# Kernel optimization log

Measured on AMD Instinct MI355X. Metric: run time of the kernel, lower is better.

Reference implementation:

```python
import jax, jax.numpy as jnp
import numpy as np

NEG_SLOPE = 0.01  # torch F.leaky_relu default


def _gcn_conv(x, edge_index, Wc, bc):
    """PyG GCNConv with add_self_loops + symmetric normalization.
    x: [N, F], edge_index: [2, E] (row=source, col=target)."""
    N = x.shape[0]
    xw = x @ Wc  # transform first, then propagate
    loop = jnp.arange(N, dtype=edge_index.dtype)
    src = jnp.concatenate([edge_index[0], loop])
    dst = jnp.concatenate([edge_index[1], loop])
    deg = jax.ops.segment_sum(jnp.ones(src.shape[0], xw.dtype), dst, num_segments=N)
    dinv = jnp.where(deg > 0, jax.lax.rsqrt(deg), 0.0)
    norm = dinv[src] * dinv[dst]  # [E+N]
    agg = jax.ops.segment_sum(norm[:, None] * xw[src], dst, num_segments=N)
    return agg + bc


def setup_inputs() -> dict:
    key = jax.random.key(0)
    ks = jax.random.split(key, 6)
    B, N, E, F, H = 8, 10000, 160000, 128, 256
    node_features = jax.random.normal(ks[0], (B, N, F), dtype=jnp.float32)
    edge_index = jax.random.randint(ks[1], (B, 2, E), 0, N, dtype=jnp.int64)
    Wc = jax.random.normal(ks[2], (F, F), dtype=jnp.float32) / np.sqrt(F)
    bc = jnp.zeros((F,), jnp.float32)
    W1 = jax.random.normal(ks[3], (F, H), dtype=jnp.float32) / np.sqrt(F)
    b1 = jnp.zeros((H,), jnp.float32)
    W2 = jax.random.normal(ks[4], (H, H), dtype=jnp.float32) / np.sqrt(H)
    b2 = jnp.zeros((H,), jnp.float32)
    return {"node_features": node_features, "edge_index": edge_index,
            "Wc": Wc, "bc": bc, "W1": W1, "b1": b1, "W2": W2, "b2": b2}


def reference(node_features, edge_index, Wc, bc, W1, b1, W2, b2):
    # vmapped per-graph GCN conv (equivalent to PyG Batch with node offsets)
    conv = jax.vmap(_gcn_conv, in_axes=(0, 0, None, None))
    x0 = node_features  # [B, N, F]
    x = jax.nn.relu(conv(x0, edge_index, Wc, bc))
    x = x + x0  # residual with raw input (batch.x)
    x = jax.nn.leaky_relu(x @ W1 + b1, NEG_SLOPE)
    x = jax.nn.leaky_relu(x @ W2 + b2, NEG_SLOPE)
    return x  # [B, N, H]
```

## Files before the change

kernel.cpp:

```cpp
#include <hip/hip_runtime.h>
#include <hip/hip_bf16.h>
#include <hip/hip_fp16.h>

#define Bn 8
#define Nn 10000
#define En 160000
#define Fn 128
#define Hn 256
#define NROW (Bn * Nn)
#define NEDGE (Bn * En)
#define TM 32

#define OFF_RS   80000
#define OFF_CUR  160004
#define OFF_BS   240004
#define OFF_BO   240320
#define OFF_EP   240832
#define WSI_END  2800832
#define WP_U16   131072
#define WP_BYTES ((size_t)WP_U16 * 2)
#define X0H_BYTES ((size_t)NROW * Fn * 2)
#define X0H_OFF  ((size_t)WSI_END * 4 + WP_BYTES)
#define WS_NEED  (X0H_OFF + X0H_BYTES)

typedef unsigned short u16;
typedef __attribute__((ext_vector_type(8))) short s16x8;
typedef __attribute__((ext_vector_type(8))) _Float16 f16x8;
typedef __attribute__((ext_vector_type(4))) float f32x4;

__device__ __forceinline__ u16 f2bf(float x) {
    unsigned u = __float_as_uint(x);
    u += 0x7FFF + ((u >> 16) & 1);
    return (u16)(u >> 16);
}
__device__ __forceinline__ float bf2f(u16 h) {
    return __uint_as_float((unsigned)h << 16);
}
__device__ __forceinline__ u16 f2h(float x) {
    _Float16 h = (_Float16)x;
    return *(u16*)&h;
}

__device__ __forceinline__ bool edge_is_i64(const int* e) {
    return e[1] == 0 && e[3] == 0;
}
__device__ __forceinline__ int eidx(const int* e, long long i, bool i64) {
    return i64 ? e[2 * i] : e[i];
}

__global__ void k_prep(int* __restrict__ deg, __half* __restrict__ x0h,
                       const float* __restrict__ x0, float* __restrict__ out,
                       const float* __restrict__ Wc, const float* __restrict__ W1,
                       const float* __restrict__ W2, u16* __restrict__ wp) {
    if (blockIdx.x < 10000) {
        int i = blockIdx.x * 256 + threadIdx.x;
        if (i < NROW) deg[i] = 1;
        if (i == 0) out[4] = 1000.0f;
        int r = i >> 5, g = i & 31;
        float4 v = *(const float4*)(x0 + ((size_t)r << 7) + (g << 2));
        __half2 a = __floats2half2_rn(v.x, v.y);
        __half2 b = __floats2half2_rn(v.z, v.w);
        uint2 u;
        u.x = *(unsigned*)&a;
        u.y = *(unsigned*)&b;
        *(uint2*)((char*)x0h + ((size_t)r << 8) + (g << 3)) = u;
    } else {
        int i = (blockIdx.x - 10000) * 256 + threadIdx.x;
        if (i < 16384) {
            int j = i & 7, l = (i >> 3) & 63;
            int nt = (i >> 9) & 7, kt = i >> 12;
            int k = kt * 32 + (l >> 4) * 8 + j;
            int n = nt * 16 + (l & 15);
            float v = Wc[(size_t)k * Fn + n];
            u16 hi = f2bf(v);
            u16 lo = f2bf(v - bf2f(hi));
            int o = (kt * 8 + nt) * 1024 + l * 8 + j;
            wp[o] = hi;
            wp[o + 512] = lo;
        } else if (i < 49152) {
            int idx = i - 16384;
            int j = idx & 7, l = (idx >> 3) & 63;
            int nt = (idx >> 9) & 15, kt = idx >> 13;
            int k = kt * 32 + (l >> 4) * 8 + j;
            int n = nt * 16 + (l & 15);
            wp[32768 + (kt * 16 + nt) * 512 + l * 8 + j] =
                f2h(W1[(size_t)k * Hn + n]);
        } else if (i < 114688) {
            int idx = i - 49152;
            int j = idx & 7, l = (idx >> 3) & 63;
            int nt = (idx >> 9) & 15, kt = idx >> 13;
            int k = kt * 32 + (l >> 4) * 8 + j;
            int n = nt * 16 + (l & 15);
            wp[65536 + (kt * 16 + nt) * 512 + l * 8 + j] =
                f2h(W2[(size_t)k * Hn + n]);
        }
    }
}

__global__ void k_deg2(const int* __restrict__ e, int* __restrict__ deg) {
    bool i64 = edge_is_i64(e);
    int b = blockIdx.x & 7;
    int p = (blockIdx.x >> 3) * 256 + threadIdx.x;
    if (p >= En / 2) return;
    int kk = p * 2;
    int d0, d1;
    if (i64) {
        int4 v = *(const int4*)(e + ((long long)(b * 2 + 1) * En + kk) * 2);
        d0 = v.x; d1 = v.z;
    } else {
        int2 v = *(const int2*)(e + (long long)(b * 2 + 1) * En + kk);
        d0 = v.x; d1 = v.y;
    }
    if ((unsigned)d0 < Nn) atomicAdd(&deg[b * Nn + d0], 1);
    if ((unsigned)d1 < Nn) atomicAdd(&deg[b * Nn + d1], 1);
}

__global__ void k_scan1(const int* __restrict__ deg,
                        int* __restrict__ row_start, int* __restrict__ bsum) {
    __shared__ int s[256];
    int i = blockIdx.x * 256 + threadIdx.x;
    int v = (i < NROW) ? (deg[i] - 1) : 0;
    s[threadIdx.x] = v;
    __syncthreads();
    for (int off = 1; off < 256; off <<= 1) {
        int t = (threadIdx.x >= off) ? s[threadIdx.x - off] : 0;
        __syncthreads();
        s[threadIdx.x] += t;
        __syncthreads();
    }
    if (i < NROW) row_start[i] = s[threadIdx.x] - v;
    if (threadIdx.x == 255) bsum[blockIdx.x] = s[255];
}

__global__ void k_scan2(const int* __restrict__ bsum, int* __restrict__ boff,
                        int* __restrict__ row_start) {
    __shared__ int s[512];
    int t = threadIdx.x;
    int v = (t < 313) ? bsum[t] : 0;
    s[t] = v;
    __syncthreads();
    for (int off = 1; off < 512; off <<= 1) {
        int u = (t >= off) ? s[t - off] : 0;
        __syncthreads();
        s[t] += u;
        __syncthreads();
    }
    boff[t] = s[t] - v;
    if (t == 511) row_start[NROW] = s[511];
}

__global__ void k_scan3(int* __restrict__ degi, float* __restrict__ dinvf,
                        int* __restrict__ row_start,
                        const int* __restrict__ boff, int* __restrict__ cursor) {
    int i = blockIdx.x * blockDim.x + threadIdx.x;
    if (i >= NROW) return;
    int v = row_start[i] + boff[i >> 8];
    row_start[i] = v;
    cursor[i] = v;
    float d = (float)degi[i];
    dinvf[i] = rsqrtf(d);
}

__global__ void k_bin2(const int* __restrict__ e, const float* __restrict__ dinv,
                       int* __restrict__ cursor, int2* __restrict__ ep) {
    bool i64 = edge_is_i64(e);
    int b = blockIdx.x & 7;
    int p = (blockIdx.x >> 3) * 256 + threadIdx.x;
    if (p >= En / 2) return;
    int kk = p * 2;
    int s0, s1, d0, d1;
    if (i64) {
        int4 sv = *(const int4*)(e + ((long long)(b * 2) * En + kk) * 2);
        int4 dv = *(const int4*)(e + ((long long)(b * 2 + 1) * En + kk) * 2);
        s0 = sv.x; s1 = sv.z; d0 = dv.x; d1 = dv.z;
    } else {
        int2 sv = *(const int2*)(e + (long long)(b * 2) * En + kk);
        int2 dv = *(const int2*)(e + (long long)(b * 2 + 1) * En + kk);
        s0 = sv.x; s1 = sv.y; d0 = dv.x; d1 = dv.y;
    }
    if ((unsigned)s0 < Nn && (unsigned)d0 < Nn) {
        int g = b * Nn + s0;
        int pos = atomicAdd(&cursor[b * Nn + d0], 1);
        ep[pos] = make_int2(g, __float_as_int(dinv[g]));
    }
    if ((unsigned)s1 < Nn && (unsigned)d1 < Nn) {
        int g = b * Nn + s1;
        int pos = atomicAdd(&cursor[b * Nn + d1], 1);
        ep[pos] = make_int2(g, __float_as_int(dinv[g]));
    }
}

__device__ __forceinline__ void g_edge_h(const __half* __restrict__ x0h, int s,
                                         float w, int lane, float& ax, float& ay) {
    __half2 h = *(const __half2*)(x0h + ((size_t)s << 7) + 2 * lane);
    float2 v = __half22float2(h);
    ax = fmaf(w, v.x, ax);
    ay = fmaf(w, v.y, ay);
}
__device__ __forceinline__ void g_pair(const __half* __restrict__ x0h,
                                       int4 pq, int lane, float& ax, float& ay) {
    g_edge_h(x0h, pq.x, __int_as_float(pq.y), lane, ax, ay);
    g_edge_h(x0h, pq.z, __int_as_float(pq.w), lane, ax, ay);
}

__global__ __launch_bounds__(256) void k_gather3(
        const __half* __restrict__ x0h, const float* __restrict__ dinv,
        const int* __restrict__ row_start, const int* __restrict__ row_end,
        const int2* __restrict__ ep, float* __restrict__ out) {
    int sb = (blockIdx.x & 7) * 2500 + (blockIdx.x >> 3);
    int wid = ((sb * 256 + (int)threadIdx.x) >> 6);
    int lane = threadIdx.x & 63;
    if (wid >= NROW) return;
    int rs = row_start[wid], re = row_end[wid];
    float wd = dinv[wid];
    float ax = 0.f, ay = 0.f;
    int j = rs;
    if (j < re && (j & 1)) {
        int2 q = ep[j];
        g_edge_h(x0h, q.x, __int_as_float(q.y), lane, ax, ay);
        ++j;
    }
    for (; j + 8 <= re; j += 8) {
        int4 p0 = *(const int4*)(ep + j);
        int4 p1 = *(const int4*)(ep + j + 2);
        int4 p2 = *(const int4*)(ep + j + 4);
        int4 p3 = *(const int4*)(ep + j + 6);
        g_pair(x0h, p0, lane, ax, ay);
        g_pair(x0h, p1, lane, ax, ay);
        g_pair(x0h, p2, lane, ax, ay);
        g_pair(x0h, p3, lane, ax, ay);
    }
    if (j + 4 <= re) {
        int4 p0 = *(const int4*)(ep + j);
        int4 p1 = *(const int4*)(ep + j + 2);
        g_pair(x0h, p0, lane, ax, ay);
        g_pair(x0h, p1, lane, ax, ay);
        j += 4;
    }
    if (j + 2 <= re) {
        int4 p0 = *(const int4*)(ep + j);
        g_pair(x0h, p0, lane, ax, ay);
        j += 2;
    }
    if (j < re) {
        int2 q = ep[j];
        g_edge_h(x0h, q.x, __int_as_float(q.y), lane, ax, ay);
    }
    g_edge_h(x0h, wid, wd, lane, ax, ay);
    float sx = wd * ax, sy = wd * ay;
    u16 h0 = f2bf(sx), h1 = f2bf(sy);
    u16 l0 = f2bf(sx - bf2f(h0)), l1 = f2bf(sy - bf2f(h1));
    unsigned* orow = (unsigned*)(out + ((size_t)wid << 8));
    orow[lane]      = (unsigned)h0 | ((unsigned)h1 << 16);
    orow[64 + lane] = (unsigned)l0 | ((unsigned)l1 << 16);
}

__global__ __launch_bounds__(256, 6) void k_fmfma(
        const float* __restrict__ x0, const u16* __restrict__ wp,
        const float* __restrict__ bc, const float* __restrict__ b1,
        const float* __restrict__ b2, float* out) {
    __shared__ __align__(16) u16 sm[13056];
    u16* rs_   = sm;
    u16* ag_hi = sm + 4352;
    u16* ag_lo = sm + 8704;
    u16* hs    = sm + 4352;

    int row0 = blockIdx.x * TM;
    int t = threadIdx.x;
    int w = t >> 6;
    int l = t & 63;
    int lr = l & 15;
    int lg = l >> 4;

#pragma unroll
    for (int it = 0; it < 4; ++it) {
        int idx = it * 256 + t;
        int r = idx >> 5, q = idx & 31;
        uint4 v = *(const uint4*)((const char*)out +
                                  ((size_t)(row0 + r) << 10) + (q << 4));
        u16* dst = (q < 16) ? (ag_hi + r * 136 + (q << 3))
                            : (ag_lo + r * 136 + ((q - 16) << 3));
        *(uint4*)dst = v;
    }
    __syncthreads();

    {
        f32x4 acc[2][2];
#pragma unroll
        for (int mi = 0; mi < 2; ++mi)
#pragma unroll
            for (int ni = 0; ni < 2; ++ni) acc[mi][ni] = (f32x4){0.f, 0.f, 0.f, 0.f};
#pragma unroll
        for (int kt = 0; kt < 4; ++kt) {
            int ka = kt * 32 + lg * 8;
            s16x8 a0h = *(const s16x8*)(ag_hi + lr * 136 + ka);
            s16x8 a0l = *(const s16x8*)(ag_lo + lr * 136 + ka);
            s16x8 a1h = *(const s16x8*)(ag_hi + (16 + lr) * 136 + ka);
            s16x8 a1l = *(const s16x8*)(ag_lo + (16 + lr) * 136 + ka);
#pragma unroll
            for (int ni = 0; ni < 2; ++ni) {
                int nt = 2 * w + ni;
                const u16* bp = wp + (kt * 8 + nt) * 1024 + l * 8;
                s16x8 bh = *(const s16x8*)(bp);
                s16x8 bl = *(const s16x8*)(bp + 512);
                acc[0][ni] = __builtin_amdgcn_mfma_f32_16x16x32_bf16(a0h, bl, acc[0][ni], 0, 0, 0);
                acc[0][ni] = __builtin_amdgcn_mfma_f32_16x16x32_bf16(a0l, bh, acc[0][ni], 0, 0, 0);
                acc[0][ni] = __builtin_amdgcn_mfma_f32_16x16x32_bf16(a0h, bh, acc[0][ni], 0, 0, 0);
                acc[1][ni] = __builtin_amdgcn_mfma_f32_16x16x32_bf16(a1h, bl, acc[1][ni], 0, 0, 0);
                acc[1][ni] = __builtin_amdgcn_mfma_f32_16x16x32_bf16(a1l, bh, acc[1][ni], 0, 0, 0);
                acc[1][ni] = __builtin_amdgcn_mfma_f32_16x16x32_bf16(a1h, bh, acc[1][ni], 0, 0, 0);
            }
        }
#pragma unroll
        for (int ni = 0; ni < 2; ++ni) {
            int col = (2 * w + ni) * 16 + lr;
            float bias = bc[col];
#pragma unroll
            for (int mi = 0; mi < 2; ++mi)
#pragma unroll
                for (int r = 0; r < 4; ++r) {
                    int row = mi * 16 + lg * 4 + r;
                    float v = acc[mi][ni][r] + bias;
                    v = fmaxf(v, 0.f) + x0[(size_t)(row0 + row) * Fn + col];
                    rs_[row * 136 + col] = f2h(v);
                }
        }
    }
    __syncthreads();

    {
        const u16* w1p = wp + 32768;
        f32x4 acc[2][4];
#pragma unroll
        for (int mi = 0; mi < 2; ++mi)
#pragma unroll
            for (int ni = 0; ni < 4; ++ni) acc[mi][ni] = (f32x4){0.f, 0.f, 0.f, 0.f};
#pragma unroll
        for (int kt = 0; kt < 4; ++kt) {
            int ka = kt * 32 + lg * 8;
            f16x8 a0 = *(const f16x8*)(rs_ + lr * 136 + ka);
            f16x8 a1 = *(const f16x8*)(rs_ + (16 + lr) * 136 + ka);
#pragma unroll
            for (int ni = 0; ni < 4; ++ni) {
                int nt = 4 * w + ni;
                f16x8 b = *(const f16x8*)(w1p + (kt * 16 + nt) * 512 + l * 8);
                acc[0][ni] = __builtin_amdgcn_mfma_f32_16x16x32_f16(a0, b, acc[0][ni], 0, 0, 0);
                acc[1][ni] = __builtin_amdgcn_mfma_f32_16x16x32_f16(a1, b, acc[1][ni], 0, 0, 0);
            }
        }
#pragma unroll
        for (int ni = 0; ni < 4; ++ni) {
            int col = (4 * w + ni) * 16 + lr;
            float bias = b1[col];
#pragma unroll
            for (int mi = 0; mi < 2; ++mi)
#pragma unroll
                for (int r = 0; r < 4; ++r) {
                    int row = mi * 16 + lg * 4 + r;
                    float v = acc[mi][ni][r] + bias;
                    v = v > 0.f ? v : 0.01f * v;
                    hs[row * 264 + col] = f2h(v);
                }
        }
    }
    __syncthreads();

    {
        const u16* w2p = wp + 65536;
        f32x4 acc[2][4];
#pragma unroll
        for (int mi = 0; mi < 2; ++mi)
#pragma unroll
            for (int ni = 0; ni < 4; ++ni) acc[mi][ni] = (f32x4){0.f, 0.f, 0.f, 0.f};
#pragma unroll
        for (int kt = 0; kt < 8; ++kt) {
            int ka = kt * 32 + lg * 8;
            f16x8 a0 = *(const f16x8*)(hs + lr * 264 + ka);
            f16x8 a1 = *(const f16x8*)(hs + (16 + lr) * 264 + ka);
#pragma unroll
            for (int ni = 0; ni < 4; ++ni) {
                int nt = 4 * w + ni;
                f16x8 b = *(const f16x8*)(w2p + (kt * 16 + nt) * 512 + l * 8);
                acc[0][ni] = __builtin_amdgcn_mfma_f32_16x16x32_f16(a0, b, acc[0][ni], 0, 0, 0);
                acc[1][ni] = __builtin_amdgcn_mfma_f32_16x16x32_f16(a1, b, acc[1][ni], 0, 0, 0);
            }
        }
#pragma unroll
        for (int ni = 0; ni < 4; ++ni) {
            int col = (4 * w + ni) * 16 + lr;
            float bias = b2[col];
#pragma unroll
            for (int mi = 0; mi < 2; ++mi)
#pragma unroll
                for (int r = 0; r < 4; ++r) {
                    int row = mi * 16 + lg * 4 + r;
                    float v = acc[mi][ni][r] + bias;
                    v = v > 0.f ? v : 0.01f * v;
                    out[((size_t)(row0 + row) << 8) + col] = v;
                }
        }
    }
}

__global__ void k_canary(float* out) {
    if (threadIdx.x == 0 && blockIdx.x == 0) out[4] = 1000.0f;
}
__global__ void k_deg_init(float* __restrict__ deg) {
    int i = blockIdx.x * blockDim.x + threadIdx.x;
    if (i < NROW) deg[i] = 1.0f;
}
__global__ void k_deg_count(const int* __restrict__ e, float* __restrict__ deg) {
    bool i64 = edge_is_i64(e);
    int i = blockIdx.x * blockDim.x + threadIdx.x;
    if (i >= NEDGE) return;
    int b = i / En, k = i - b * En;
    int dst = eidx(e, (long long)(b * 2 + 1) * En + k, i64);
    if ((unsigned)dst < Nn) atomicAdd(&deg[b * Nn + dst], 1.0f);
}
__global__ void k_dinv(float* __restrict__ deg) {
    int i = blockIdx.x * blockDim.x + threadIdx.x;
    if (i < NROW) deg[i] = rsqrtf(deg[i]);
}
__global__ void k_agg_init(const float* __restrict__ x0,
                           const float* __restrict__ dinv,
                           float* __restrict__ out) {
    int i = blockIdx.x * blockDim.x + threadIdx.x;
    if (i >= NROW * Fn) return;
    int r = i >> 7;
    int c = i & 127;
    float dv = dinv[r];
    out[((size_t)r << 8) + c] = dv * dv * x0[i];
}
__global__ void k_scatter(const int* __restrict__ e,
                          const float* __restrict__ dinv,
                          const float* __restrict__ x0,
                          float* __restrict__ out) {
    bool i64 = edge_is_i64(e);
    long long gid = (long long)blockIdx.x * blockDim.x + threadIdx.x;
    int eid = (int)(gid >> 6);
    int lane = (int)(gid & 63);
    if (eid >= NEDGE) return;
    int b = eid / En, k = eid - b * En;
    int src = eidx(e, (long long)(b * 2) * En + k, i64);
    int dst = eidx(e, (long long)(b * 2 + 1) * En + k, i64);
    if ((unsigned)src >= Nn || (unsigned)dst >= Nn) return;
    float nrm = dinv[b * Nn + src] * dinv[b * Nn + dst];
    const float2 vf =
        *(const float2*)(x0 + ((size_t)(b * Nn + src) << 7) + 2 * lane);
    float* p = out + ((size_t)(b * Nn + dst) << 8) + 2 * lane;
    atomicAdd(p, nrm * vf.x);
    atomicAdd(p + 1, nrm * vf.y);
}

__global__ __launch_bounds__(256, 3) void k_fused(
        const float* __restrict__ x0,
        const float* __restrict__ Wc, const float* __restrict__ bc,
        const float* __restrict__ W1, const float* __restrict__ b1,
        const float* __restrict__ W2, const float* __restrict__ b2,
        float* out) {
    __shared__ float smem[12352];
    float (*rs)[Fn + 1] = (float (*)[Fn + 1])smem;
    float (*ag)[Fn + 1] = (float (*)[Fn + 1])(smem + 4128);
    float (*hs)[Hn + 1] = (float (*)[Hn + 1])(smem + 4128);

    int row0 = blockIdx.x * TM;
    int t = threadIdx.x;
    int tx = t & 31;
    int ty = t >> 5;
    int ra = ty * 4;

    for (int i = t; i < TM * Fn; i += 256) {
        int r = i >> 7, c = i & 127;
        ag[r][c] = out[((size_t)(row0 + r) << 8) + c];
    }
    __syncthreads();
    {
        float acc[4][4] = {};
#pragma unroll 4
        for (int k = 0; k < Fn; ++k) {
            float a0 = ag[ra + 0][k], a1 = ag[ra + 1][k],
                  a2 = ag[ra + 2][k], a3 = ag[ra + 3][k];
            const float4 b = *(const float4*)(Wc + k * Fn + tx * 4);
            acc[0][0] = fmaf(a0, b.x, acc[0][0]); acc[0][1] = fmaf(a0, b.y, acc[0][1]);
            acc[0][2] = fmaf(a0, b.z, acc[0][2]); acc[0][3] = fmaf(a0, b.w, acc[0][3]);
            acc[1][0] = fmaf(a1, b.x, acc[1][0]); acc[1][1] = fmaf(a1, b.y, acc[1][1]);
            acc[1][2] = fmaf(a1, b.z, acc[1][2]); acc[1][3] = fmaf(a1, b.w, acc[1][3]);
            acc[2][0] = fmaf(a2, b.x, acc[2][0]); acc[2][1] = fmaf(a2, b.y, acc[2][1]);
            acc[2][2] = fmaf(a2, b.z, acc[2][2]); acc[2][3] = fmaf(a2, b.w, acc[2][3]);
            acc[3][0] = fmaf(a3, b.x, acc[3][0]); acc[3][1] = fmaf(a3, b.y, acc[3][1]);
            acc[3][2] = fmaf(a3, b.z, acc[3][2]); acc[3][3] = fmaf(a3, b.w, acc[3][3]);
        }
        const float4 bcv = *(const float4*)(bc + tx * 4);
        __syncthreads();
#pragma unroll
        for (int i = 0; i < 4; ++i) {
            const float4 xv =
                *(const float4*)(x0 + (size_t)(row0 + ra + i) * Fn + tx * 4);
            rs[ra + i][tx * 4 + 0] = fmaxf(acc[i][0] + bcv.x, 0.f) + xv.x;
            rs[ra + i][tx * 4 + 1] = fmaxf(acc[i][1] + bcv.y, 0.f) + xv.y;
            rs[ra + i][tx * 4 + 2] = fmaxf(acc[i][2] + bcv.z, 0.f) + xv.z;
            rs[ra + i][tx * 4 + 3] = fmaxf(acc[i][3] + bcv.w, 0.f) + xv.w;
        }
    }
    __syncthreads();
    {
        float acc[4][8] = {};
#pragma unroll 2
        for (int k = 0; k < Fn; ++k) {
            float a0 = rs[ra + 0][k], a1 = rs[ra + 1][k],
                  a2 = rs[ra + 2][k], a3 = rs[ra + 3][k];
            const float4 p0 = *(const float4*)(W1 + k * Hn + tx * 8);
            const float4 p1 = *(const float4*)(W1 + k * Hn + tx * 8 + 4);
#pragma unroll
            for (int i = 0; i < 4; ++i) {
                float a = (i == 0) ? a0 : (i == 1) ? a1 : (i == 2) ? a2 : a3;
                acc[i][0] = fmaf(a, p0.x, acc[i][0]); acc[i][1] = fmaf(a, p0.y, acc[i][1]);
                acc[i][2] = fmaf(a, p0.z, acc[i][2]); acc[i][3] = fmaf(a, p0.w, acc[i][3]);
                acc[i][4] = fmaf(a, p1.x, acc[i][4]); acc[i][5] = fmaf(a, p1.y, acc[i][5]);
                acc[i][6] = fmaf(a, p1.z, acc[i][6]); acc[i][7] = fmaf(a, p1.w, acc[i][7]);
            }
        }
        const float4 b1a = *(const float4*)(b1 + tx * 8);
        const float4 b1b = *(const float4*)(b1 + tx * 8 + 4);
        float bias[8] = {b1a.x, b1a.y, b1a.z, b1a.w, b1b.x, b1b.y, b1b.z, b1b.w};
#pragma unroll
        for (int i = 0; i < 4; ++i)
#pragma unroll
            for (int j = 0; j < 8; ++j) {
                float h = acc[i][j] + bias[j];
                hs[ra + i][tx * 8 + j] = h > 0.f ? h : 0.01f * h;
            }
    }
    __syncthreads();
    {
        float acc[4][8] = {};
#pragma unroll 2
        for (int k = 0; k < Hn; ++k) {
            float a0 = hs[ra + 0][k], a1 = hs[ra + 1][k],
                  a2 = hs[ra + 2][k], a3 = hs[ra + 3][k];
            const float4 p0 = *(const float4*)(W2 + k * Hn + tx * 8);
            const float4 p1 = *(const float4*)(W2 + k * Hn + tx * 8 + 4);
#pragma unroll
            for (int i = 0; i < 4; ++i) {
                float a = (i == 0) ? a0 : (i == 1) ? a1 : (i == 2) ? a2 : a3;
                acc[i][0] = fmaf(a, p0.x, acc[i][0]); acc[i][1] = fmaf(a, p0.y, acc[i][1]);
                acc[i][2] = fmaf(a, p0.z, acc[i][2]); acc[i][3] = fmaf(a, p0.w, acc[i][3]);
                acc[i][4] = fmaf(a, p1.x, acc[i][4]); acc[i][5] = fmaf(a, p1.y, acc[i][5]);
                acc[i][6] = fmaf(a, p1.z, acc[i][6]); acc[i][7] = fmaf(a, p1.w, acc[i][7]);
            }
        }
        const float4 b2a = *(const float4*)(b2 + tx * 8);
        const float4 b2b = *(const float4*)(b2 + tx * 8 + 4);
        float bias[8] = {b2a.x, b2a.y, b2a.z, b2a.w, b2b.x, b2b.y, b2b.z, b2b.w};
#pragma unroll
        for (int i = 0; i < 4; ++i) {
            float o[8];
#pragma unroll
            for (int j = 0; j < 8; ++j) {
                float v = acc[i][j] + bias[j];
                o[j] = v > 0.f ? v : 0.01f * v;
            }
            float* dst = out + ((size_t)(row0 + ra + i) << 8) + tx * 8;
            *(float4*)(dst)     = make_float4(o[0], o[1], o[2], o[3]);
            *(float4*)(dst + 4) = make_float4(o[4], o[5], o[6], o[7]);
        }
    }
}

extern "C" void kernel_launch(void* const* d_in, const int* in_sizes, int n_in,
                              void* d_out, int out_size, void* d_ws, size_t ws_size,
                              hipStream_t stream) {
    const float* x0 = (const float*)d_in[0];
    const int*   ed = (const int*)d_in[1];
    const float* Wc = (const float*)d_in[2];
    const float* bc = (const float*)d_in[3];
    const float* W1 = (const float*)d_in[4];
    const float* b1 = (const float*)d_in[5];
    const float* W2 = (const float*)d_in[6];
    const float* b2 = (const float*)d_in[7];

    float* out = (float*)d_out;
    int*   wsi = (int*)d_ws;
    float* wsf = (float*)d_ws;

    if (ws_size >= WS_NEED) {
        int*    degi      = wsi;
        float*  dinv      = wsf;
        int*    row_start = wsi + OFF_RS;
        int*    cursor    = wsi + OFF_CUR;
        int*    bsum      = wsi + OFF_BS;
        int*    boff      = wsi + OFF_BO;
        int2*   ep        = (int2*)(wsi + OFF_EP);
        u16*    wp        = (u16*)(wsi + WSI_END);
        __half* x0h       = (__half*)((char*)d_ws + X0H_OFF);

        int epb = 8 * ((En / 2 + 255) / 256);
        k_prep<<<10448, 256, 0, stream>>>(degi, x0h, x0, out, Wc, W1, W2, wp);
        k_deg2<<<epb, 256, 0, stream>>>(ed, degi);
        k_scan1<<<313, 256, 0, stream>>>(degi, row_start, bsum);
        k_scan2<<<1, 512, 0, stream>>>(bsum, boff, row_start);
        k_scan3<<<313, 256, 0, stream>>>(degi, dinv, row_start, boff, cursor);
        k_bin2<<<epb, 256, 0, stream>>>(ed, dinv, cursor, ep);
        k_gather3<<<NROW / 4, 256, 0, stream>>>(
            x0h, dinv, row_start, cursor, ep, out);
        k_fmfma<<<NROW / TM, 256, 0, stream>>>(x0, wp, bc, b1, b2, out);
    } else {
        float* deg = wsf;
        k_canary<<<1, 64, 0, stream>>>(out);
        k_deg_init<<<(NROW + 255) / 256, 256, 0, stream>>>(deg);
        k_deg_count<<<(NEDGE + 255) / 256, 256, 0, stream>>>(ed, deg);
        k_dinv<<<(NROW + 255) / 256, 256, 0, stream>>>(deg);
        k_agg_init<<<(NROW * Fn + 255) / 256, 256, 0, stream>>>(x0, deg, out);
        long long sthreads = (long long)NEDGE * 64;
        k_scatter<<<(int)((sthreads + 255) / 256), 256, 0, stream>>>(ed, deg, x0, out);
        k_fused<<<NROW / TM, 256, 0, stream>>>(x0, Wc, bc, W1, b1, W2, b2, out);
    }
}
```

Baseline: 333.1 us.

## Fuse edge gather into MFMA MLP kernel and stage aggregation in LDS

Merges the per-row edge gather into the fused GEMM kernel so each block aggregates its 32 rows directly into shared memory as bf16 hi/lo pairs, removing the global write and re-read of the aggregated features and one kernel launch. The residual input is now taken from the fp16 copy of x0 loaded into LDS instead of fp32 x0 from global memory. Block indices are remapped per XCD into contiguous row ranges. In exchange, each wave processes 8 rows serially with fewer total blocks, which may reduce latency hiding for the irregular gathers, and the residual uses reduced precision.

```diff
diff --git a/kernel.cpp b/kernel.cpp
--- a/kernel.cpp
+++ b/kernel.cpp
@@ -203,60 +203,10 @@
     g_edge_h(x0h, pq.z, __int_as_float(pq.w), lane, ax, ay);
 }
 
-__global__ __launch_bounds__(256) void k_gather3(
+__global__ __launch_bounds__(256, 6) void k_gfm(
         const __half* __restrict__ x0h, const float* __restrict__ dinv,
         const int* __restrict__ row_start, const int* __restrict__ row_end,
-        const int2* __restrict__ ep, float* __restrict__ out) {
-    int sb = (blockIdx.x & 7) * 2500 + (blockIdx.x >> 3);
-    int wid = ((sb * 256 + (int)threadIdx.x) >> 6);
-    int lane = threadIdx.x & 63;
-    if (wid >= NROW) return;
-    int rs = row_start[wid], re = row_end[wid];
-    float wd = dinv[wid];
-    float ax = 0.f, ay = 0.f;
-    int j = rs;
-    if (j < re && (j & 1)) {
-        int2 q = ep[j];
-        g_edge_h(x0h, q.x, __int_as_float(q.y), lane, ax, ay);
-        ++j;
-    }
-    for (; j + 8 <= re; j += 8) {
-        int4 p0 = *(const int4*)(ep + j);
-        int4 p1 = *(const int4*)(ep + j + 2);
-        int4 p2 = *(const int4*)(ep + j + 4);
-        int4 p3 = *(const int4*)(ep + j + 6);
-        g_pair(x0h, p0, lane, ax, ay);
-        g_pair(x0h, p1, lane, ax, ay);
-        g_pair(x0h, p2, lane, ax, ay);
-        g_pair(x0h, p3, lane, ax, ay);
-    }
-    if (j + 4 <= re) {
-        int4 p0 = *(const int4*)(ep + j);
-        int4 p1 = *(const int4*)(ep + j + 2);
-        g_pair(x0h, p0, lane, ax, ay);
-        g_pair(x0h, p1, lane, ax, ay);
-        j += 4;
-    }
-    if (j + 2 <= re) {
-        int4 p0 = *(const int4*)(ep + j);
-        g_pair(x0h, p0, lane, ax, ay);
-        j += 2;
-    }
-    if (j < re) {
-        int2 q = ep[j];
-        g_edge_h(x0h, q.x, __int_as_float(q.y), lane, ax, ay);
-    }
-    g_edge_h(x0h, wid, wd, lane, ax, ay);
-    float sx = wd * ax, sy = wd * ay;
-    u16 h0 = f2bf(sx), h1 = f2bf(sy);
-    u16 l0 = f2bf(sx - bf2f(h0)), l1 = f2bf(sy - bf2f(h1));
-    unsigned* orow = (unsigned*)(out + ((size_t)wid << 8));
-    orow[lane]      = (unsigned)h0 | ((unsigned)h1 << 16);
-    orow[64 + lane] = (unsigned)l0 | ((unsigned)l1 << 16);
-}
-
-__global__ __launch_bounds__(256, 6) void k_fmfma(
-        const float* __restrict__ x0, const u16* __restrict__ wp,
+        const int2* __restrict__ ep, const u16* __restrict__ wp,
         const float* __restrict__ bc, const float* __restrict__ b1,
         const float* __restrict__ b2, float* out) {
     __shared__ __align__(16) u16 sm[13056];
@@ -265,7 +215,10 @@
     u16* ag_lo = sm + 8704;
     u16* hs    = sm + 4352;
 
-    int row0 = blockIdx.x * TM;
+    int xcd = blockIdx.x & 7, ii = blockIdx.x >> 3;
+    int wg = (xcd < 4 ? xcd * 313 : 1252 + (xcd - 4) * 312) + ii;
+    int row0 = wg * TM;
+
     int t = threadIdx.x;
     int w = t >> 6;
     int l = t & 63;
@@ -273,14 +226,58 @@
     int lg = l >> 4;
 
 #pragma unroll
-    for (int it = 0; it < 4; ++it) {
+    for (int it = 0; it < 2; ++it) {
         int idx = it * 256 + t;
-        int r = idx >> 5, q = idx & 31;
-        uint4 v = *(const uint4*)((const char*)out +
-                                  ((size_t)(row0 + r) << 10) + (q << 4));
-        u16* dst = (q < 16) ? (ag_hi + r * 136 + (q << 3))
-                            : (ag_lo + r * 136 + ((q - 16) << 3));
-        *(uint4*)dst = v;
+        int r = idx >> 4, c = idx & 15;
+        *(uint4*)(rs_ + r * 136 + (c << 3)) =
+            *(const uint4*)(x0h + ((size_t)(row0 + r) << 7) + (c << 3));
+    }
+
+#pragma unroll 1
+    for (int rr = 0; rr < 8; ++rr) {
+        int r = w * 8 + rr;
+        int wid = row0 + r;
+        int rs = row_start[wid], re = row_end[wid];
+        float wd = dinv[wid];
+        float ax = 0.f, ay = 0.f;
+        int j = rs;
+        if (j < re && (j & 1)) {
+            int2 q = ep[j];
+            g_edge_h(x0h, q.x, __int_as_float(q.y), l, ax, ay);
+            ++j;
+        }
+        for (; j + 8 <= re; j += 8) {
+            int4 p0 = *(const int4*)(ep + j);
+            int4 p1 = *(const int4*)(ep + j + 2);
+            int4 p2 = *(const int4*)(ep + j + 4);
+            int4 p3 = *(const int4*)(ep + j + 6);
+            g_pair(x0h, p0, l, ax, ay);
+            g_pair(x0h, p1, l, ax, ay);
+            g_pair(x0h, p2, l, ax, ay);
+            g_pair(x0h, p3, l, ax, ay);
+        }
+        if (j + 4 <= re) {
+            int4 p0 = *(const int4*)(ep + j);
+            int4 p1 = *(const int4*)(ep + j + 2);
+            g_pair(x0h, p0, l, ax, ay);
+            g_pair(x0h, p1, l, ax, ay);
+            j += 4;
+        }
+        if (j + 2 <= re) {
+            int4 p0 = *(const int4*)(ep + j);
+            g_pair(x0h, p0, l, ax, ay);
+            j += 2;
+        }
+        if (j < re) {
+            int2 q = ep[j];
+            g_edge_h(x0h, q.x, __int_as_float(q.y), l, ax, ay);
+        }
+        g_edge_h(x0h, wid, wd, l, ax, ay);
+        float sx = wd * ax, sy = wd * ay;
+        u16 h0 = f2bf(sx), h1 = f2bf(sy);
+        u16 l0 = f2bf(sx - bf2f(h0)), l1 = f2bf(sy - bf2f(h1));
+        ((unsigned*)ag_hi)[r * 68 + l] = (unsigned)h0 | ((unsigned)h1 << 16);
+        ((unsigned*)ag_lo)[r * 68 + l] = (unsigned)l0 | ((unsigned)l1 << 16);
     }
     __syncthreads();
 
@@ -320,8 +317,9 @@
 #pragma unroll
                 for (int r = 0; r < 4; ++r) {
                     int row = mi * 16 + lg * 4 + r;
+                    float xr = (float)*(const _Float16*)(rs_ + row * 136 + col);
                     float v = acc[mi][ni][r] + bias;
-                    v = fmaxf(v, 0.f) + x0[(size_t)(row0 + row) * Fn + col];
+                    v = fmaxf(v, 0.f) + xr;
                     rs_[row * 136 + col] = f2h(v);
                 }
         }
@@ -601,9 +599,8 @@
         k_scan2<<<1, 512, 0, stream>>>(bsum, boff, row_start);
         k_scan3<<<313, 256, 0, stream>>>(degi, dinv, row_start, boff, cursor);
         k_bin2<<<epb, 256, 0, stream>>>(ed, dinv, cursor, ep);
-        k_gather3<<<NROW / 4, 256, 0, stream>>>(
-            x0h, dinv, row_start, cursor, ep, out);
-        k_fmfma<<<NROW / TM, 256, 0, stream>>>(x0, wp, bc, b1, b2, out);
+        k_gfm<<<NROW / TM, 256, 0, stream>>>(
+            x0h, dinv, row_start, cursor, ep, wp, bc, b1, b2, out);
     } else {
         float* deg = wsf;
         k_canary<<<1, 64, 0, stream>>>(out);
```

Result: faster. 313.8 us (-5.8%).
